# Performance work log

Measured on AMD Instinct MI355X. Metric: run time of the kernel, lower is better.

The kernel has to match this reference:

```python
import jax, jax.numpy as jnp
import numpy as np

STATE_MASS = 4.0
EPS = 1e-5
LOW_RANK_SCALE = 0.1  # _LOW_RANK_SCALE_INIT


def _ln(x, g, b):
    mu = jnp.mean(x, axis=-1, keepdims=True)
    var = jnp.var(x, axis=-1, keepdims=True)
    return (x - mu) * jax.lax.rsqrt(var + EPS) * g + b


def _signed_abs_softmax(s, axis=-1):
    s = jnp.nan_to_num(s)
    return jnp.sign(s) * jax.nn.softmax(jnp.abs(s), axis=axis)


def _signed_softmax_state(st):
    st = jnp.nan_to_num(st)
    return jnp.sign(st) * jax.nn.softmax(jnp.abs(st), axis=-1) * STATE_MASS


def _low_rank_scores(dst, src, Ut_w, Ut_b, Us_w, Us_b, w):
    # bilinear low-rank pairwise: score[b,i,j] = sum_r (dst_i Ut)_r * w_r * (src_j Us)_r
    pt = dst @ Ut_w + Ut_b                      # [B,Nd,R]
    ps = src @ Us_w + Us_b                      # [B,Ns,R]
    return jnp.einsum('bir,r,bjr->bij', pt, w * LOW_RANK_SCALE, ps)


def _gather_rows(x, idx):
    # x: [B,N,...], idx: [B,M,K] -> [B,M,K,...] (per-batch gather, no NxM broadcast)
    return jax.vmap(lambda xi, ii: xi[ii])(x, idx)


def setup_inputs() -> dict:
    key = jax.random.key(0)
    ks = jax.random.split(key, 8)
    B, S, D, M, R = 16, 2048, 512, 256, 64
    std = 0.02
    return {
        'token_val': jax.random.normal(ks[0], (B, S, D), jnp.float32),
        'token_state': jax.random.normal(ks[1], (B, S), jnp.float32),
        'init_state': jax.random.normal(ks[2], (M,), jnp.float32) * std,
        'init_val': jax.random.normal(ks[3], (M, D), jnp.float32) * std,
        'rUs_w': jax.random.normal(ks[4], (D, R), jnp.float32) * std,
        'rUs_b': jnp.zeros((R,), jnp.float32),
        'rUt_w': jax.random.normal(ks[5], (D, R), jnp.float32) * std,
        'rUt_b': jnp.zeros((R,), jnp.float32),
        'r_w': jnp.ones((R,), jnp.float32),
        'pUs_w': jax.random.normal(ks[6], (D, R), jnp.float32) * std,
        'pUs_b': jnp.zeros((R,), jnp.float32),
        'pUt_w': jax.random.normal(ks[7], (D, R), jnp.float32) * std,
        'pUt_b': jnp.zeros((R,), jnp.float32),
        'p_w': jnp.ones((R,), jnp.float32),
        'ln_g': jnp.ones((D,), jnp.float32),
        'ln_b': jnp.zeros((D,), jnp.float32),
        'topk': 16,
    }


def reference(token_val, token_state, init_state, init_val,
              rUs_w, rUs_b, rUt_w, rUt_b, r_w,
              pUs_w, pUs_b, pUt_w, pUt_b, p_w,
              ln_g, ln_b, topk):
    B = token_val.shape[0]
    M, D = init_val.shape

    # _MemoryLevel.initialize
    mem_state = _signed_softmax_state(jnp.broadcast_to(init_state, (B, M)))
    mem_val = _ln(jnp.broadcast_to(init_val, (B, M, D)), ln_g, ln_b)

    # ---- SparseTransition (write): route tokens -> slots, top-k sources/slot ----
    scores = _low_rank_scores(mem_val, token_val, rUt_w, rUt_b, rUs_w, rUs_b, r_w)  # [B,M,S]
    _, idx = jax.lax.top_k(jnp.abs(scores), topk)              # [B,M,K]
    sel = jnp.take_along_axis(scores, idx, axis=-1)            # [B,M,K]
    edges = _signed_abs_softmax(sel, axis=-1)                  # signed-abs-softmax over edges
    v_sel = _gather_rows(token_val, idx)                       # [B,M,K,D]
    s_sel = _gather_rows(token_state, idx)                     # [B,M,K]
    mem_val = mem_val + jnp.einsum('bmk,bmkd->bmd', edges, v_sel)   # merge_mode='add'
    mem_state = mem_state + jnp.einsum('bmk,bmk->bm', edges, s_sel)
    mem_state = _signed_softmax_state(mem_state)
    mem_val = _ln(mem_val, ln_g, ln_b)

    # ---- SparsePropagation within slots: state-weighted top-k edges, residual ----
    pscores = _low_rank_scores(mem_val, mem_val, pUt_w, pUt_b, pUs_w, pUs_b, p_w)   # [B,M,M]
    pscores = pscores * mem_state[:, None, :]                  # state_weight_edges
    _, pidx = jax.lax.top_k(jnp.abs(pscores), topk)            # [B,M,K]
    psel = jnp.take_along_axis(pscores, pidx, axis=-1)
    pe = _signed_abs_softmax(psel, axis=-1)
    pv = _gather_rows(mem_val, pidx)                           # [B,M,K,D]
    pst = _gather_rows(mem_state, pidx)                        # [B,M,K]
    mem_val = mem_val + jnp.einsum('bmk,bmkd->bmd', pe, pv)    # residual=True
    mem_state = mem_state + jnp.einsum('bmk,bmk->bm', pe, pst)
    mem_state = _signed_softmax_state(mem_state)
    mem_val = _ln(mem_val, ln_g, ln_b)
    return mem_val
```

## Files before the change

### kernel.cpp

```cpp
#include <hip/hip_runtime.h>
#include <hip/hip_bf16.h>
#include <math.h>

#define BB 16
#define SS 2048
#define DD 512
#define MM 256
#define RR 64
#define KK 16
#define GPAD 68

__device__ __forceinline__ float wave_sum(float v) {
#pragma unroll
  for (int off = 32; off > 0; off >>= 1) v += __shfl_xor(v, off);
  return v;
}

__device__ __forceinline__ float sgnf(float v) {
  return (v > 0.f) ? 1.f : ((v < 0.f) ? -1.f : 0.f);
}

__global__ __launch_bounds__(256) void k_init(
    const float* __restrict__ init_val, const float* __restrict__ ln_g,
    const float* __restrict__ ln_b, const float* __restrict__ rUt_w,
    const float* __restrict__ rUt_b, const float* __restrict__ r_w,
    float* __restrict__ mv0, float* __restrict__ pt0) {
  int m = blockIdx.x, t = threadIdx.x;
  __shared__ float row[DD];
  __shared__ float red[8];
  float x0 = init_val[m * DD + t];
  float x1 = init_val[m * DD + t + 256];
  float s = wave_sum(x0 + x1);
  float sq = wave_sum(x0 * x0 + x1 * x1);
  if ((t & 63) == 0) { red[t >> 6] = s; red[4 + (t >> 6)] = sq; }
  __syncthreads();
  float mean = (red[0] + red[1] + red[2] + red[3]) * (1.0f / DD);
  float var = (red[4] + red[5] + red[6] + red[7]) * (1.0f / DD) - mean * mean;
  float rs = rsqrtf(var + 1e-5f);
  float n0 = (x0 - mean) * rs * ln_g[t] + ln_b[t];
  float n1 = (x1 - mean) * rs * ln_g[t + 256] + ln_b[t + 256];
  mv0[m * DD + t] = n0;
  mv0[m * DD + t + 256] = n1;
  row[t] = n0;
  row[t + 256] = n1;
  __syncthreads();
  if (t < RR) {
    float acc = rUt_b[t];
    for (int d = 0; d < DD; ++d) acc += row[d] * rUt_w[d * RR + t];
    pt0[m * RR + t] = acc * r_w[t] * 0.1f;
  }
}

__global__ __launch_bounds__(256) void k_state_softmax(
    const float* __restrict__ in, float* __restrict__ out) {
  int b = blockIdx.x, t = threadIdx.x;
  __shared__ float red[4];
  float v = in[b * MM + t];
  float a = fabsf(v);
  float mx = a;
#pragma unroll
  for (int off = 32; off > 0; off >>= 1) mx = fmaxf(mx, __shfl_xor(mx, off));
  if ((t & 63) == 0) red[t >> 6] = mx;
  __syncthreads();
  mx = fmaxf(fmaxf(red[0], red[1]), fmaxf(red[2], red[3]));
  __syncthreads();
  float e = expf(a - mx);
  float ssum = wave_sum(e);
  if ((t & 63) == 0) red[t >> 6] = ssum;
  __syncthreads();
  ssum = red[0] + red[1] + red[2] + red[3];
  out[b * MM + t] = sgnf(v) * e / ssum * 4.0f;
}

__global__ __launch_bounds__(128) void k_ps(
    const float* __restrict__ A, const float* __restrict__ W,
    const float* __restrict__ bias, float* __restrict__ C0,
    float* __restrict__ C1, float* __restrict__ C2, float* __restrict__ C3) {
  __shared__ float Ast[32][128];
  __shared__ float Ws[32][RR];
  int t = threadIdx.x;
  int cg = t & 7;
  int rg = t >> 3;
  int q = blockIdx.x >> 8;
  int row0 = (blockIdx.x & 255) * 128;
  int k0 = q * 128;
  float* C = (q == 0) ? C0 : (q == 1) ? C1 : (q == 2) ? C2 : C3;
  float acc[8][8] = {};
  for (int c = 0; c < 4; ++c) {
    int kc = k0 + c * 32;
    float4 ra[8];
#pragma unroll
    for (int i = 0; i < 8; ++i)
      ra[i] = *reinterpret_cast<const float4*>(
          &A[(size_t)(row0 + t) * DD + kc + i * 4]);
    float4 rw[4];
#pragma unroll
    for (int i = 0; i < 4; ++i) {
      int slot = i * 128 + t;
      rw[i] = *reinterpret_cast<const float4*>(
          &W[(size_t)(kc + (slot >> 4)) * RR + (slot & 15) * 4]);
    }
    __syncthreads();
#pragma unroll
    for (int i = 0; i < 8; ++i) {
      Ast[i * 4 + 0][t] = ra[i].x;
      Ast[i * 4 + 1][t] = ra[i].y;
      Ast[i * 4 + 2][t] = ra[i].z;
      Ast[i * 4 + 3][t] = ra[i].w;
    }
#pragma unroll
    for (int i = 0; i < 4; ++i) {
      int slot = i * 128 + t;
      *reinterpret_cast<float4*>(&Ws[slot >> 4][(slot & 15) * 4]) = rw[i];
    }
    __syncthreads();
#pragma unroll
    for (int k = 0; k < 32; ++k) {
      float4 a0 = *reinterpret_cast<const float4*>(&Ast[k][rg * 8]);
      float4 a1 = *reinterpret_cast<const float4*>(&Ast[k][rg * 8 + 4]);
      float4 w0 = *reinterpret_cast<const float4*>(&Ws[k][cg * 8]);
      float4 w1 = *reinterpret_cast<const float4*>(&Ws[k][cg * 8 + 4]);
      float av[8] = {a0.x, a0.y, a0.z, a0.w, a1.x, a1.y, a1.z, a1.w};
      float wv[8] = {w0.x, w0.y, w0.z, w0.w, w1.x, w1.y, w1.z, w1.w};
#pragma unroll
      for (int r = 0; r < 8; ++r)
#pragma unroll
        for (int cc = 0; cc < 8; ++cc) acc[r][cc] += av[r] * wv[cc];
    }
  }
  float bvx[8];
#pragma unroll
  for (int cc = 0; cc < 8; ++cc) bvx[cc] = (q == 0) ? bias[cg * 8 + cc] : 0.f;
#pragma unroll
  for (int r = 0; r < 8; ++r) {
    int rr = row0 + rg * 8 + r;
    float4 o0, o1;
    o0.x = acc[r][0] + bvx[0]; o0.y = acc[r][1] + bvx[1];
    o0.z = acc[r][2] + bvx[2]; o0.w = acc[r][3] + bvx[3];
    o1.x = acc[r][4] + bvx[4]; o1.y = acc[r][5] + bvx[5];
    o1.z = acc[r][6] + bvx[6]; o1.w = acc[r][7] + bvx[7];
    *reinterpret_cast<float4*>(&C[(size_t)rr * RR + cg * 8]) = o0;
    *reinterpret_cast<float4*>(&C[(size_t)rr * RR + cg * 8 + 4]) = o1;
  }
}

template <bool TRANS_OUT>
__device__ __forceinline__ void gemm_body(
    const float* __restrict__ A, const float* __restrict__ W,
    const float* __restrict__ bias, const float* __restrict__ colscale,
    float csmul, const float* __restrict__ rowscale, float* __restrict__ C,
    int row0, float (*Ast)[GPAD], float (*Ws)[GPAD]) {
  int tid = threadIdx.x;
  int ty = tid >> 4, tx = tid & 15;
  float acc[4][4] = {};
  for (int kc = 0; kc < DD; kc += 32) {
#pragma unroll
    for (int i = 0; i < 2; ++i) {
      int s4 = i * 256 + tid;
      int r = s4 >> 3;
      int k4 = s4 & 7;
      float4 v = *reinterpret_cast<const float4*>(
          &A[(size_t)(row0 + r) * DD + kc + k4 * 4]);
      Ast[k4 * 4 + 0][r] = v.x;
      Ast[k4 * 4 + 1][r] = v.y;
      Ast[k4 * 4 + 2][r] = v.z;
      Ast[k4 * 4 + 3][r] = v.w;
    }
#pragma unroll
    for (int i = 0; i < 2; ++i) {
      int s4 = i * 256 + tid;
      int r = s4 >> 4;
      int c4 = s4 & 15;
      float4 v = *reinterpret_cast<const float4*>(
          &W[(size_t)(kc + r) * RR + c4 * 4]);
      *reinterpret_cast<float4*>(&Ws[r][c4 * 4]) = v;
    }
    __syncthreads();
#pragma unroll
    for (int k = 0; k < 32; ++k) {
      float4 a4 = *reinterpret_cast<const float4*>(&Ast[k][ty * 4]);
      float4 w4 = *reinterpret_cast<const float4*>(&Ws[k][tx * 4]);
      acc[0][0] += a4.x * w4.x; acc[0][1] += a4.x * w4.y;
      acc[0][2] += a4.x * w4.z; acc[0][3] += a4.x * w4.w;
      acc[1][0] += a4.y * w4.x; acc[1][1] += a4.y * w4.y;
      acc[1][2] += a4.y * w4.z; acc[1][3] += a4.y * w4.w;
      acc[2][0] += a4.z * w4.x; acc[2][1] += a4.z * w4.y;
      acc[2][2] += a4.z * w4.z; acc[2][3] += a4.z * w4.w;
      acc[3][0] += a4.w * w4.x; acc[3][1] += a4.w * w4.y;
      acc[3][2] += a4.w * w4.z; acc[3][3] += a4.w * w4.w;
    }
    __syncthreads();
  }
#pragma unroll
  for (int i = 0; i < 4; ++i) {
    int rr = row0 + ty * 4 + i;
    float rsc = rowscale ? rowscale[rr] : 1.f;
#pragma unroll
    for (int j = 0; j < 4; ++j) {
      int cc = tx * 4 + j;
      float v = acc[i][j] + bias[cc];
      if (colscale) v *= colscale[cc] * csmul;
      v *= rsc;
      if (TRANS_OUT) {
        C[((size_t)(rr >> 8) * RR + cc) * MM + (rr & 255)] = v;
      } else {
        C[(size_t)rr * RR + cc] = v;
      }
    }
  }
}

__global__ __launch_bounds__(256) void k_gemm_pair(
    const float* __restrict__ mv1, const float* __restrict__ pUt_w,
    const float* __restrict__ pUt_b, const float* __restrict__ p_w,
    const float* __restrict__ pUs_w, const float* __restrict__ pUs_b,
    const float* __restrict__ ms1, float* __restrict__ pt1,
    float* __restrict__ ps1T) {
  __shared__ float Ast[32][GPAD];
  __shared__ float Ws[32][GPAD];
  if (blockIdx.x < 64) {
    gemm_body<false>(mv1, pUt_w, pUt_b, p_w, 0.1f, nullptr, pt1,
                     blockIdx.x * 64, Ast, Ws);
  } else {
    gemm_body<true>(mv1, pUs_w, pUs_b, nullptr, 1.f, ms1, ps1T,
                    (blockIdx.x - 64) * 64, Ast, Ws);
  }
}

#define PSW 144
__device__ __forceinline__ int psw(int j) { return j + ((j >> 5) << 2); }

__global__ __launch_bounds__(256) void k_scores(
    const float* __restrict__ pt0, const float* __restrict__ ps0,
    const float* __restrict__ ps1, const float* __restrict__ ps2,
    const float* __restrict__ ps3, float* __restrict__ scores) {
  __shared__ float PtT[RR][128];
  __shared__ float PsT[RR][PSW];
  int t = threadIdx.x;
  int b = blockIdx.z;
  int m0 = blockIdx.y * 128;
  int j0 = blockIdx.x * 128;
#pragma unroll
  for (int ii = 0; ii < 2; ++ii) {
    int slot = ii * 256 + t;
    int tm4 = slot >> 4, tk4 = slot & 15;
    const float* base = pt0 + (size_t)(m0 + tm4 * 4) * RR + tk4 * 4;
    float4 v0 = *reinterpret_cast<const float4*>(base);
    float4 v1 = *reinterpret_cast<const float4*>(base + RR);
    float4 v2 = *reinterpret_cast<const float4*>(base + 2 * RR);
    float4 v3 = *reinterpret_cast<const float4*>(base + 3 * RR);
    float4 w;
    w.x = v0.x; w.y = v1.x; w.z = v2.x; w.w = v3.x;
    *reinterpret_cast<float4*>(&PtT[tk4 * 4 + 0][tm4 * 4]) = w;
    w.x = v0.y; w.y = v1.y; w.z = v2.y; w.w = v3.y;
    *reinterpret_cast<float4*>(&PtT[tk4 * 4 + 1][tm4 * 4]) = w;
    w.x = v0.z; w.y = v1.z; w.z = v2.z; w.w = v3.z;
    *reinterpret_cast<float4*>(&PtT[tk4 * 4 + 2][tm4 * 4]) = w;
    w.x = v0.w; w.y = v1.w; w.z = v2.w; w.w = v3.w;
    *reinterpret_cast<float4*>(&PtT[tk4 * 4 + 3][tm4 * 4]) = w;
  }
#pragma unroll
  for (int ii = 0; ii < 2; ++ii) {
    int slot = ii * 256 + t;
    int jt = slot >> 4, kt = slot & 15;
    size_t off = ((size_t)b * SS + j0 + jt * 4) * RR + kt * 4;
    float4 v0, v1, v2, v3;
    {
      const float* p0 = ps0 + off;
      const float* p1 = ps1 + off;
      const float* p2 = ps2 + off;
      const float* p3 = ps3 + off;
#pragma unroll
      for (int rr2 = 0; rr2 < 4; ++rr2) {
        float4 a = *reinterpret_cast<const float4*>(p0 + rr2 * RR);
        float4 bq = *reinterpret_cast<const float4*>(p1 + rr2 * RR);
        float4 cq = *reinterpret_cast<const float4*>(p2 + rr2 * RR);
        float4 dq = *reinterpret_cast<const float4*>(p3 + rr2 * RR);
        float4 r;
        r.x = a.x + bq.x + cq.x + dq.x;
        r.y = a.y + bq.y + cq.y + dq.y;
        r.z = a.z + bq.z + cq.z + dq.z;
        r.w = a.w + bq.w + cq.w + dq.w;
        if (rr2 == 0) v0 = r; else if (rr2 == 1) v1 = r;
        else if (rr2 == 2) v2 = r; else v3 = r;
      }
    }
    int jc = psw(jt * 4);
    float4 w;
    w.x = v0.x; w.y = v1.x; w.z = v2.x; w.w = v3.x;
    *reinterpret_cast<float4*>(&PsT[kt * 4 + 0][jc]) = w;
    w.x = v0.y; w.y = v1.y; w.z = v2.y; w.w = v3.y;
    *reinterpret_cast<float4*>(&PsT[kt * 4 + 1][jc]) = w;
    w.x = v0.z; w.y = v1.z; w.z = v2.z; w.w = v3.z;
    *reinterpret_cast<float4*>(&PsT[kt * 4 + 2][jc]) = w;
    w.x = v0.w; w.y = v1.w; w.z = v2.w; w.w = v3.w;
    *reinterpret_cast<float4*>(&PsT[kt * 4 + 3][jc]) = w;
  }
  __syncthreads();
  int jg = t & 15;
  int mg = t >> 4;
  int jlo = psw(jg * 8);
  float acc[8][8] = {};
#pragma unroll
  for (int k = 0; k < RR; ++k) {
    float4 a0 = *reinterpret_cast<const float4*>(&PtT[k][mg * 8]);
    float4 a1 = *reinterpret_cast<const float4*>(&PtT[k][mg * 8 + 4]);
    float4 w0 = *reinterpret_cast<const float4*>(&PsT[k][jlo]);
    float4 w1 = *reinterpret_cast<const float4*>(&PsT[k][jlo + 4]);
    float av[8] = {a0.x, a0.y, a0.z, a0.w, a1.x, a1.y, a1.z, a1.w};
    float wv[8] = {w0.x, w0.y, w0.z, w0.w, w1.x, w1.y, w1.z, w1.w};
#pragma unroll
    for (int r = 0; r < 8; ++r)
#pragma unroll
      for (int cc = 0; cc < 8; ++cc) acc[r][cc] += av[r] * wv[cc];
  }
  float* obase =
      scores + (size_t)b * MM * SS + (size_t)(m0 + mg * 8) * SS + j0 + jg * 8;
#pragma unroll
  for (int r = 0; r < 8; ++r) {
    float4 o0, o1;
    o0.x = acc[r][0]; o0.y = acc[r][1]; o0.z = acc[r][2]; o0.w = acc[r][3];
    o1.x = acc[r][4]; o1.y = acc[r][5]; o1.z = acc[r][6]; o1.w = acc[r][7];
    *reinterpret_cast<float4*>(obase + (size_t)r * SS) = o0;
    *reinterpret_cast<float4*>(obase + (size_t)r * SS + 4) = o1;
  }
}

__global__ __launch_bounds__(256) void k_write(
    const float* __restrict__ scores, const float* __restrict__ token_val,
    const float* __restrict__ token_state, const float* __restrict__ mv0,
    const float* __restrict__ ms0, const float* __restrict__ ln_g,
    const float* __restrict__ ln_b, float* __restrict__ mv1,
    float* __restrict__ ms_w) {
  int t = threadIdx.x;
  int wave = t >> 6, lane = t & 63;
  int i = blockIdx.x;
  int slot = i >> 3;
  int b = 2 * (i & 7) + (slot >> 6);
  int m = (slot & 63) * 4 + wave;
  int row = b * MM + m;
  __shared__ float srl[4][SS];
  __shared__ int selj_sh[4][KK];
  float4* srl4 = reinterpret_cast<float4*>(&srl[wave][0]);
  const float* srow = scores + (size_t)row * SS;
  unsigned au[32];
  unsigned maxa = 0u;
#pragma unroll
  for (int ch = 0; ch < 8; ++ch) {
    float4 q = *reinterpret_cast<const float4*>(srow + (ch * 64 + lane) * 4);
    srl4[ch * 64 + lane] = q;
    au[ch * 4 + 0] = __float_as_uint(q.x) & 0x7fffffffu;
    au[ch * 4 + 1] = __float_as_uint(q.y) & 0x7fffffffu;
    au[ch * 4 + 2] = __float_as_uint(q.z) & 0x7fffffffu;
    au[ch * 4 + 3] = __float_as_uint(q.w) & 0x7fffffffu;
    maxa = max(maxa, max(max(au[ch * 4], au[ch * 4 + 1]),
                         max(au[ch * 4 + 2], au[ch * 4 + 3])));
  }
#pragma unroll
  for (int off = 32; off > 0; off >>= 1)
    maxa = max(maxa, (unsigned)__shfl_xor((int)maxa, off));
  unsigned lo = 0u, hi = maxa, thr = 0u;
  bool early = false;
  while (lo < hi) {
    unsigned mid = lo + ((hi - lo + 1u) >> 1);
    int cnt = 0;
#pragma unroll
    for (int c = 0; c < 32; ++c) cnt += __popcll(__ballot(au[c] >= mid));
    if (cnt == KK) { thr = mid; early = true; break; }
    if (cnt > KK) lo = mid; else hi = mid - 1u;
  }
  if (!early) thr = lo;
  unsigned long long ltmask = (1ull << lane) - 1ull;
  int s = 0;
  unsigned tiemask = 0u;
#pragma unroll
  for (int c = 0; c < 32; ++c) {
    bool sg = early ? (au[c] >= thr) : (au[c] > thr);
    unsigned long long mk = __ballot(sg);
    if (sg)
      selj_sh[wave][s + __popcll(mk & ltmask)] =
          (c >> 2) * 256 + lane * 4 + (c & 3);
    s += __popcll(mk);
    if (!early && au[c] == thr) tiemask |= 1u << c;
  }
  int taken = s;
  while (taken < KK) {
    int myj = 0x7fffffff;
#pragma unroll
    for (int c = 0; c < 32; ++c)
      if ((tiemask >> c) & 1u) {
        int j = (c >> 2) * 256 + lane * 4 + (c & 3);
        myj = min(myj, j);
      }
    int wj = myj;
#pragma unroll
    for (int off = 32; off > 0; off >>= 1) wj = min(wj, __shfl_xor(wj, off));
    if (wj == 0x7fffffff) break;
    if (((wj >> 2) & 63) == lane) tiemask &= ~(1u << (((wj >> 8) << 2) | (wj & 3)));
    if (lane == 0) selj_sh[wave][taken] = wj;
    ++taken;
  }
  int js[KK];
  float es[KK];
#pragma unroll
  for (int k = 0; k < KK; ++k) {
    js[k] = selj_sh[wave][k];
    es[k] = srl[wave][js[k]];
  }
  float mx = 0.f;
#pragma unroll
  for (int k = 0; k < KK; ++k) mx = fmaxf(mx, fabsf(es[k]));
  float ssum = 0.f;
#pragma unroll
  for (int k = 0; k < KK; ++k) {
    float ex = expf(fabsf(es[k]) - mx);
    ssum += ex;
    es[k] = sgnf(es[k]) * ex;
  }
  float inv = 1.f / ssum;
  int dbase = lane * 8;
  const float* m0row = mv0 + m * DD + dbase;
  float4 a0 = *reinterpret_cast<const float4*>(m0row);
  float4 a1 = *reinterpret_cast<const float4*>(m0row + 4);
  float acc[8] = {a0.x, a0.y, a0.z, a0.w, a1.x, a1.y, a1.z, a1.w};
  float stacc = 0.f;
#pragma unroll
  for (int k = 0; k < KK; ++k) {
    float e = es[k] * inv;
    const float* tv = token_val + ((size_t)b * SS + js[k]) * DD + dbase;
    float4 u0 = *reinterpret_cast<const float4*>(tv);
    float4 u1 = *reinterpret_cast<const float4*>(tv + 4);
    acc[0] += e * u0.x; acc[1] += e * u0.y; acc[2] += e * u0.z; acc[3] += e * u0.w;
    acc[4] += e * u1.x; acc[5] += e * u1.y; acc[6] += e * u1.z; acc[7] += e * u1.w;
    stacc += e * token_state[(size_t)b * SS + js[k]];
  }
  if (lane == 0) ms_w[row] = ms0[m] + stacc;
  float s1 = 0.f, s2 = 0.f;
#pragma unroll
  for (int c = 0; c < 8; ++c) { s1 += acc[c]; s2 += acc[c] * acc[c]; }
  s1 = wave_sum(s1);
  s2 = wave_sum(s2);
  float mean = s1 * (1.0f / DD);
  float var = s2 * (1.0f / DD) - mean * mean;
  float rs = rsqrtf(var + 1e-5f);
  float4 g0 = *reinterpret_cast<const float4*>(ln_g + dbase);
  float4 g1 = *reinterpret_cast<const float4*>(ln_g + dbase + 4);
  float4 b0v = *reinterpret_cast<const float4*>(ln_b + dbase);
  float4 b1v = *reinterpret_cast<const float4*>(ln_b + dbase + 4);
  float4 o0, o1;
  o0.x = (acc[0] - mean) * rs * g0.x + b0v.x;
  o0.y = (acc[1] - mean) * rs * g0.y + b0v.y;
  o0.z = (acc[2] - mean) * rs * g0.z + b0v.z;
  o0.w = (acc[3] - mean) * rs * g0.w + b0v.w;
  o1.x = (acc[4] - mean) * rs * g1.x + b1v.x;
  o1.y = (acc[5] - mean) * rs * g1.y + b1v.y;
  o1.z = (acc[6] - mean) * rs * g1.z + b1v.z;
  o1.w = (acc[7] - mean) * rs * g1.w + b1v.w;
  float* orow = mv1 + (size_t)row * DD + dbase;
  *reinterpret_cast<float4*>(orow) = o0;
  *reinterpret_cast<float4*>(orow + 4) = o1;
}

__global__ __launch_bounds__(256, 4) void k_prop(
    const float* __restrict__ pt1, const float* __restrict__ ps1T,
    const float* __restrict__ mv1, const float* __restrict__ ln_g,
    const float* __restrict__ ln_b, float* __restrict__ out) {
  int t = threadIdx.x;
  int wave = t >> 6, lane = t & 63;
  int row = blockIdx.x * 4 + wave;
  int b = row >> 8, m = row & 255;
  __shared__ int selj_sh[4][KK];
  __shared__ float selv_sh[4][KK];
  float ptval = pt1[(size_t)row * RR + lane];
  const float* pB = ps1T + (size_t)b * RR * MM + lane * 4;
  float sc[4] = {0.f, 0.f, 0.f, 0.f};
#pragma unroll 8
  for (int r = 0; r < RR; ++r) {
    float w = __shfl(ptval, r);
    float4 pv = *reinterpret_cast<const float4*>(pB + r * MM);
    sc[0] += w * pv.x; sc[1] += w * pv.y; sc[2] += w * pv.z; sc[3] += w * pv.w;
  }
  int jbase = lane * 4;
  unsigned au[4];
#pragma unroll
  for (int c = 0; c < 4; ++c) au[c] = __float_as_uint(sc[c]) & 0x7fffffffu;
  unsigned lo = 0u, hi = 0x7f800000u, thr = 0u;
  bool early = false;
  while (lo < hi) {
    unsigned mid = lo + ((hi - lo + 1u) >> 1);
    int cnt = 0;
#pragma unroll
    for (int c = 0; c < 4; ++c) cnt += __popcll(__ballot(au[c] >= mid));
    if (cnt == KK) { thr = mid; early = true; break; }
    if (cnt > KK) lo = mid; else hi = mid - 1u;
  }
  if (!early) thr = lo;
  unsigned long long ltmask = (1ull << lane) - 1ull;
  int s = 0;
  unsigned tiemask = 0u;
#pragma unroll
  for (int c = 0; c < 4; ++c) {
    bool sg = early ? (au[c] >= thr) : (au[c] > thr);
    unsigned long long mk = __ballot(sg);
    if (sg) {
      int slot = s + __popcll(mk & ltmask);
      selj_sh[wave][slot] = jbase + c;
      selv_sh[wave][slot] = sc[c];
    }
    s += __popcll(mk);
    if (!early && au[c] == thr) tiemask |= 1u << c;
  }
  int taken = s;
  while (taken < KK) {
    int myj = 0x7fffffff;
#pragma unroll
    for (int c = 0; c < 4; ++c)
      if ((tiemask >> c) & 1u) myj = min(myj, jbase + c);
    int wj = myj;
#pragma unroll
    for (int off = 32; off > 0; off >>= 1) wj = min(wj, __shfl_xor(wj, off));
    if (wj == 0x7fffffff) break;
    if (wj >= jbase && wj < jbase + 4) {
      tiemask &= ~(1u << (wj - jbase));
      selv_sh[wave][taken] = sc[wj - jbase];
      if (lane == (wj >> 2)) selj_sh[wave][taken] = wj;
    }
    ++taken;
  }
  int js[KK];
  float es[KK];
#pragma unroll
  for (int k = 0; k < KK; ++k) { js[k] = selj_sh[wave][k]; es[k] = selv_sh[wave][k]; }
  float mx = 0.f;
#pragma unroll
  for (int k = 0; k < KK; ++k) mx = fmaxf(mx, fabsf(es[k]));
  float ssum = 0.f;
#pragma unroll
  for (int k = 0; k < KK; ++k) {
    float ex = expf(fabsf(es[k]) - mx);
    ssum += ex;
    es[k] = sgnf(es[k]) * ex;
  }
  float inv = 1.f / ssum;
  int dbase = lane * 8;
  const float* mrow = mv1 + (size_t)row * DD + dbase;
  float4 a0 = *reinterpret_cast<const float4*>(mrow);
  float4 a1 = *reinterpret_cast<const float4*>(mrow + 4);
  float acc[8] = {a0.x, a0.y, a0.z, a0.w, a1.x, a1.y, a1.z, a1.w};
#pragma unroll
  for (int k = 0; k < KK; ++k) {
    float e = es[k] * inv;
    const float* pv = mv1 + ((size_t)b * MM + js[k]) * DD + dbase;
    float4 u0 = *reinterpret_cast<const float4*>(pv);
    float4 u1 = *reinterpret_cast<const float4*>(pv + 4);
    acc[0] += e * u0.x; acc[1] += e * u0.y; acc[2] += e * u0.z; acc[3] += e * u0.w;
    acc[4] += e * u1.x; acc[5] += e * u1.y; acc[6] += e * u1.z; acc[7] += e * u1.w;
  }
  float s1 = 0.f, s2 = 0.f;
#pragma unroll
  for (int c = 0; c < 8; ++c) { s1 += acc[c]; s2 += acc[c] * acc[c]; }
  s1 = wave_sum(s1);
  s2 = wave_sum(s2);
  float mean = s1 * (1.0f / DD);
  float var = s2 * (1.0f / DD) - mean * mean;
  float rs = rsqrtf(var + 1e-5f);
  float4 g0 = *reinterpret_cast<const float4*>(ln_g + dbase);
  float4 g1 = *reinterpret_cast<const float4*>(ln_g + dbase + 4);
  float4 b0v = *reinterpret_cast<const float4*>(ln_b + dbase);
  float4 b1v = *reinterpret_cast<const float4*>(ln_b + dbase + 4);
  float4 o0, o1;
  o0.x = (acc[0] - mean) * rs * g0.x + b0v.x;
  o0.y = (acc[1] - mean) * rs * g0.y + b0v.y;
  o0.z = (acc[2] - mean) * rs * g0.z + b0v.z;
  o0.w = (acc[3] - mean) * rs * g0.w + b0v.w;
  o1.x = (acc[4] - mean) * rs * g1.x + b1v.x;
  o1.y = (acc[5] - mean) * rs * g1.y + b1v.y;
  o1.z = (acc[6] - mean) * rs * g1.z + b1v.z;
  o1.w = (acc[7] - mean) * rs * g1.w + b1v.w;
  float* orow = out + (size_t)row * DD + dbase;
  *reinterpret_cast<float4*>(orow) = o0;
  *reinterpret_cast<float4*>(orow + 4) = o1;
}

extern "C" void kernel_launch(void* const* d_in, const int* in_sizes, int n_in,
                              void* d_out, int out_size, void* d_ws,
                              size_t ws_size, hipStream_t stream) {
  const float* token_val = (const float*)d_in[0];
  const float* token_state = (const float*)d_in[1];
  const float* init_state = (const float*)d_in[2];
  const float* init_val = (const float*)d_in[3];
  const float* rUs_w = (const float*)d_in[4];
  const float* rUs_b = (const float*)d_in[5];
  const float* rUt_w = (const float*)d_in[6];
  const float* rUt_b = (const float*)d_in[7];
  const float* r_w = (const float*)d_in[8];
  const float* pUs_w = (const float*)d_in[9];
  const float* pUs_b = (const float*)d_in[10];
  const float* pUt_w = (const float*)d_in[11];
  const float* pUt_b = (const float*)d_in[12];
  const float* p_w = (const float*)d_in[13];
  const float* ln_g = (const float*)d_in[14];
  const float* ln_b = (const float*)d_in[15];
  float* out = (float*)d_out;

  float* ws = (float*)d_ws;
  float* mv0 = ws;    ws += MM * DD;
  float* pt0 = ws;    ws += MM * RR;
  float* ms0 = ws;    ws += MM;
  float* ps = ws;     ws += (size_t)BB * SS * RR;
  float* scores = ws; ws += (size_t)BB * MM * SS;
  float* mv1 = ws;    ws += (size_t)BB * MM * DD;
  float* ms_w = ws;   ws += BB * MM;
  float* ms1 = ws;    ws += BB * MM;
  float* pt1 = ws;    ws += (size_t)BB * MM * RR;
  float* ps1T = ws;   ws += (size_t)BB * RR * MM;
  float* ps2 = ws;    ws += (size_t)BB * SS * RR;
  float* psB = mv1;
  float* psD = out;

  k_init<<<MM, 256, 0, stream>>>(init_val, ln_g, ln_b, rUt_w, rUt_b, r_w, mv0, pt0);
  k_state_softmax<<<1, 256, 0, stream>>>(init_state, ms0);
  k_ps<<<1024, 128, 0, stream>>>(token_val, rUs_w, rUs_b, ps, psB, ps2, psD);
  dim3 gs(SS / 128, MM / 128, BB);
  k_scores<<<gs, 256, 0, stream>>>(pt0, ps, psB, ps2, psD, scores);
  k_write<<<(BB * MM) / 4, 256, 0, stream>>>(scores, token_val, token_state,
                                             mv0, ms0, ln_g, ln_b, mv1, ms_w);
  k_state_softmax<<<BB, 256, 0, stream>>>(ms_w, ms1);
  k_gemm_pair<<<128, 256, 0, stream>>>(mv1, pUt_w, pUt_b, p_w, pUs_w, pUs_b,
                                       ms1, pt1, ps1T);
  k_prop<<<(BB * MM) / 4, 256, 0, stream>>>(pt1, ps1T, mv1, ln_g, ln_b, out);
}
```

Baseline: 167.2 us.

## Retile k_ps projection GEMM into smaller 64-thread blocks with register-held weights

Restructures the token-to-rank projection GEMM (B*S x 512 by 512 x 64, split four ways along K) from 1024 blocks of 128 threads with 128-row tiles into 4096 single-wave blocks with 32-row tiles. Weights are now read straight from global into registers per 8-wide K chunk instead of being staged in shared memory, and only a small A tile goes through LDS. The aim is to raise occupancy and parallelism across CUs and cut LDS traffic. In exchange, each thread does less register reuse (4x8 instead of 8x8 outputs), the weights are re-read far more often through cache, and there are more barriers per K step.

```diff
diff --git a/kernel.cpp b/kernel.cpp
--- a/kernel.cpp
+++ b/kernel.cpp
@@ -72,73 +72,62 @@
   out[b * MM + t] = sgnf(v) * e / ssum * 4.0f;
 }
 
-__global__ __launch_bounds__(128) void k_ps(
+__global__ __launch_bounds__(64) void k_ps(
     const float* __restrict__ A, const float* __restrict__ W,
     const float* __restrict__ bias, float* __restrict__ C0,
     float* __restrict__ C1, float* __restrict__ C2, float* __restrict__ C3) {
-  __shared__ float Ast[32][128];
-  __shared__ float Ws[32][RR];
+  __shared__ float Ast[8][32];
   int t = threadIdx.x;
+  int rg = t >> 3;
   int cg = t & 7;
-  int rg = t >> 3;
-  int q = blockIdx.x >> 8;
-  int row0 = (blockIdx.x & 255) * 128;
+  int q = blockIdx.x >> 10;
+  int rt = blockIdx.x & 1023;
+  int row0 = rt * 32;
   int k0 = q * 128;
   float* C = (q == 0) ? C0 : (q == 1) ? C1 : (q == 2) ? C2 : C3;
-  float acc[8][8] = {};
-  for (int c = 0; c < 4; ++c) {
-    int kc = k0 + c * 32;
-    float4 ra[8];
-#pragma unroll
-    for (int i = 0; i < 8; ++i)
-      ra[i] = *reinterpret_cast<const float4*>(
-          &A[(size_t)(row0 + t) * DD + kc + i * 4]);
-    float4 rw[4];
-#pragma unroll
-    for (int i = 0; i < 4; ++i) {
-      int slot = i * 128 + t;
-      rw[i] = *reinterpret_cast<const float4*>(
-          &W[(size_t)(kc + (slot >> 4)) * RR + (slot & 15) * 4]);
+  int lr = t >> 1;
+  int ks = (t & 1) * 4;
+  float acc[4][8] = {};
+  for (int ch = 0; ch < 16; ++ch) {
+    int kc = k0 + ch * 8;
+    float4 av4 = *reinterpret_cast<const float4*>(
+        &A[(size_t)(row0 + lr) * DD + kc + ks]);
+    float4 wlo[8], whi[8];
+#pragma unroll
+    for (int j = 0; j < 8; ++j) {
+      const float* wr = W + (size_t)(kc + j) * RR + cg * 8;
+      wlo[j] = *reinterpret_cast<const float4*>(wr);
+      whi[j] = *reinterpret_cast<const float4*>(wr + 4);
     }
     __syncthreads();
-#pragma unroll
-    for (int i = 0; i < 8; ++i) {
-      Ast[i * 4 + 0][t] = ra[i].x;
-      Ast[i * 4 + 1][t] = ra[i].y;
-      Ast[i * 4 + 2][t] = ra[i].z;
-      Ast[i * 4 + 3][t] = ra[i].w;
-    }
-#pragma unroll
-    for (int i = 0; i < 4; ++i) {
-      int slot = i * 128 + t;
-      *reinterpret_cast<float4*>(&Ws[slot >> 4][(slot & 15) * 4]) = rw[i];
-    }
+    Ast[ks + 0][lr] = av4.x;
+    Ast[ks + 1][lr] = av4.y;
+    Ast[ks + 2][lr] = av4.z;
+    Ast[ks + 3][lr] = av4.w;
     __syncthreads();
 #pragma unroll
-    for (int k = 0; k < 32; ++k) {
-      float4 a0 = *reinterpret_cast<const float4*>(&Ast[k][rg * 8]);
-      float4 a1 = *reinterpret_cast<const float4*>(&Ast[k][rg * 8 + 4]);
-      float4 w0 = *reinterpret_cast<const float4*>(&Ws[k][cg * 8]);
-      float4 w1 = *reinterpret_cast<const float4*>(&Ws[k][cg * 8 + 4]);
-      float av[8] = {a0.x, a0.y, a0.z, a0.w, a1.x, a1.y, a1.z, a1.w};
-      float wv[8] = {w0.x, w0.y, w0.z, w0.w, w1.x, w1.y, w1.z, w1.w};
-#pragma unroll
-      for (int r = 0; r < 8; ++r)
-#pragma unroll
-        for (int cc = 0; cc < 8; ++cc) acc[r][cc] += av[r] * wv[cc];
+    for (int j = 0; j < 8; ++j) {
+      float4 a4 = *reinterpret_cast<const float4*>(&Ast[j][rg * 4]);
+      float wv[8] = {wlo[j].x, wlo[j].y, wlo[j].z, wlo[j].w,
+                     whi[j].x, whi[j].y, whi[j].z, whi[j].w};
+      float av[4] = {a4.x, a4.y, a4.z, a4.w};
+#pragma unroll
+      for (int i = 0; i < 4; ++i)
+#pragma unroll
+        for (int c = 0; c < 8; ++c) acc[i][c] += av[i] * wv[c];
     }
   }
   float bvx[8];
 #pragma unroll
-  for (int cc = 0; cc < 8; ++cc) bvx[cc] = (q == 0) ? bias[cg * 8 + cc] : 0.f;
-#pragma unroll
-  for (int r = 0; r < 8; ++r) {
-    int rr = row0 + rg * 8 + r;
+  for (int c = 0; c < 8; ++c) bvx[c] = (q == 0) ? bias[cg * 8 + c] : 0.f;
+#pragma unroll
+  for (int i = 0; i < 4; ++i) {
+    int rr = row0 + rg * 4 + i;
     float4 o0, o1;
-    o0.x = acc[r][0] + bvx[0]; o0.y = acc[r][1] + bvx[1];
-    o0.z = acc[r][2] + bvx[2]; o0.w = acc[r][3] + bvx[3];
-    o1.x = acc[r][4] + bvx[4]; o1.y = acc[r][5] + bvx[5];
-    o1.z = acc[r][6] + bvx[6]; o1.w = acc[r][7] + bvx[7];
+    o0.x = acc[i][0] + bvx[0]; o0.y = acc[i][1] + bvx[1];
+    o0.z = acc[i][2] + bvx[2]; o0.w = acc[i][3] + bvx[3];
+    o1.x = acc[i][4] + bvx[4]; o1.y = acc[i][5] + bvx[5];
+    o1.z = acc[i][6] + bvx[6]; o1.w = acc[i][7] + bvx[7];
     *reinterpret_cast<float4*>(&C[(size_t)rr * RR + cg * 8]) = o0;
     *reinterpret_cast<float4*>(&C[(size_t)rr * RR + cg * 8 + 4]) = o1;
   }
@@ -620,7 +609,7 @@
 
   k_init<<<MM, 256, 0, stream>>>(init_val, ln_g, ln_b, rUt_w, rUt_b, r_w, mv0, pt0);
   k_state_softmax<<<1, 256, 0, stream>>>(init_state, ms0);
-  k_ps<<<1024, 128, 0, stream>>>(token_val, rUs_w, rUs_b, ps, psB, ps2, psD);
+  k_ps<<<4096, 64, 0, stream>>>(token_val, rUs_w, rUs_b, ps, psB, ps2, psD);
   dim3 gs(SS / 128, MM / 128, BB);
   k_scores<<<gs, 256, 0, stream>>>(pt0, ps, psB, ps2, psD, scores);
   k_write<<<(BB * MM) / 4, 256, 0, stream>>>(scores, token_val, token_state,
```

Result: slower. 173.1 us (+3.5%).
